# Kernel optimization log

Measured on AMD Instinct MI355X. Metric: run time of the kernel, lower is better.

The kernel has to match this reference:

```python
import jax, jax.numpy as jnp
import numpy as np

N_NODES = 100000

def sage_conv(x, edge_index, W_l, b_l, W_r):
    # PyG SAGEConv (aggr='mean'): out = lin_l(mean_{j in N(i)} x_j) + lin_r(x_i)
    src = edge_index[0]  # message source nodes
    dst = edge_index[1]  # aggregation target nodes
    msgs = x[src]                                   # [E, F] gather
    agg = jax.ops.segment_sum(msgs, dst, num_segments=N_NODES)      # [N, F]
    cnt = jax.ops.segment_sum(jnp.ones((edge_index.shape[1],), x.dtype), dst,
                              num_segments=N_NODES)                 # [N]
    mean = agg / jnp.clip(cnt, 1.0)[:, None]
    return mean @ W_l.T + b_l + x @ W_r.T


def setup_inputs() -> dict:
    key = jax.random.key(0)
    ks = jax.random.split(key, 8)
    num_features, hid, num_classes = 500, 8, 10
    n_edges = 3200000
    x = jax.random.normal(ks[0], (N_NODES, num_features), dtype=jnp.float32)
    edge_index = jax.random.randint(ks[1], (2, n_edges), 0, N_NODES, dtype=jnp.int64)
    def lin(k, fan_in, fan_out):
        bound = 1.0 / np.sqrt(fan_in)
        return jax.random.uniform(k, (fan_out, fan_in), jnp.float32, -bound, bound)
    W1_l = lin(ks[2], num_features, hid)
    b1_l = jax.random.uniform(ks[3], (hid,), jnp.float32, -1/np.sqrt(num_features), 1/np.sqrt(num_features))
    W1_r = lin(ks[4], num_features, hid)
    W2_l = lin(ks[5], hid, num_classes)
    b2_l = jax.random.uniform(ks[6], (num_classes,), jnp.float32, -1/np.sqrt(hid), 1/np.sqrt(hid))
    W2_r = lin(ks[7], hid, num_classes)
    return {"x": x, "edge_index": edge_index,
            "W1_l": W1_l, "b1_l": b1_l, "W1_r": W1_r,
            "W2_l": W2_l, "b2_l": b2_l, "W2_r": W2_r}


def reference(x, edge_index, W1_l, b1_l, W1_r, W2_l, b2_l, W2_r):
    # eval mode: dropout is a no-op
    h = sage_conv(x, edge_index, W1_l, b1_l, W1_r)
    h = jax.nn.elu(h)
    out = sage_conv(h, edge_index, W2_l, b2_l, W2_r)
    return jax.nn.log_softmax(out, axis=1)
```

## Files before the change

### kernel.cpp

```cpp
#include <hip/hip_runtime.h>
#include <hip/hip_bf16.h>
#include <math.h>


#define NBKT_MAX 1600
#define P_BLOCKS 256
#define BSH 6
#define BSZ 64
#define SEG_CAP 4096

typedef float f4v __attribute__((ext_vector_type(4)));
typedef float f32x4 __attribute__((ext_vector_type(4)));
typedef unsigned u32x4 __attribute__((ext_vector_type(4)));
typedef __bf16 bf16x8 __attribute__((ext_vector_type(8)));

__device__ __forceinline__ unsigned f2bf(float f) {
    unsigned u = __float_as_uint(f);
    return (u + 0x7FFFu + ((u >> 16) & 1u)) >> 16;
}
__device__ __forceinline__ float bflo(unsigned w) { return __uint_as_float(w << 16); }
__device__ __forceinline__ float bfhi(unsigned w) { return __uint_as_float(w & 0xFFFF0000u); }

__device__ __forceinline__ unsigned pk2(float lo, float hi) {
    union { __hip_bfloat162 h; unsigned u; } c;
    c.h = __float22bfloat162_rn(make_float2(lo, hi));
    return c.u;
}

__global__ __launch_bounds__(256) void proj1_kernel(
    const float* __restrict__ x,
    const float* __restrict__ W1l,
    const float* __restrict__ W1r,
    unsigned short* __restrict__ yab,
    float* __restrict__ yr,
    int N)
{
    __shared__ __align__(16) unsigned short wls[16 * 520];
    for (int idx = threadIdx.x; idx < 16 * 520; idx += 256) {
        int m = idx / 520, k = idx - m * 520;
        float v = 0.f;
        if (k < 500) v = (m < 8) ? W1l[m * 500 + k] : W1r[(m - 8) * 500 + k];
        wls[idx] = (unsigned short)f2bf(v);
    }
    __syncthreads();

    const int lane = threadIdx.x & 63;
    const int wv   = threadIdx.x >> 6;
    const int tile = blockIdx.x * 4 + wv;
    if (tile * 16 >= N) return;

    const int m  = lane & 15;
    const int kg = lane >> 4;
    const int nodeA = min(tile * 16 + m, N - 1);
    const float* xrow = x + (size_t)nodeA * 500 + kg * 8;
    const unsigned short* wrow = wls + m * 520 + kg * 8;

    union { u32x4 u; bf16x8 b; } af, bf;
    f32x4 acc = {0.f, 0.f, 0.f, 0.f};
    const f4v zero4 = {0.f, 0.f, 0.f, 0.f};

    #pragma unroll 5
    for (int s = 0; s < 15; ++s) {
        f4v xa = *reinterpret_cast<const f4v*>(xrow + s * 32);
        f4v xb = *reinterpret_cast<const f4v*>(xrow + s * 32 + 4);
        af.u.x = pk2(xa.x, xa.y); af.u.y = pk2(xa.z, xa.w);
        af.u.z = pk2(xb.x, xb.y); af.u.w = pk2(xb.z, xb.w);
        bf.b = *reinterpret_cast<const bf16x8*>(wrow + s * 32);
        acc = __builtin_amdgcn_mfma_f32_16x16x32_bf16(af.b, bf.b, acc, 0, 0, 0);
    }
    {
        const int k0 = 480 + kg * 8;
        f4v xa = (k0 + 4 <= 500) ? *reinterpret_cast<const f4v*>(xrow + 480) : zero4;
        f4v xb = (k0 + 8 <= 500) ? *reinterpret_cast<const f4v*>(xrow + 484) : zero4;
        af.u.x = pk2(xa.x, xa.y); af.u.y = pk2(xa.z, xa.w);
        af.u.z = pk2(xb.x, xb.y); af.u.w = pk2(xb.z, xb.w);
        bf.b = *reinterpret_cast<const bf16x8*>(wrow + 480);
        acc = __builtin_amdgcn_mfma_f32_16x16x32_bf16(af.b, bf.b, acc, 0, 0, 0);
    }

    const int ndb = tile * 16 + kg * 4;
    #pragma unroll
    for (int r = 0; r < 4; ++r) {
        int nd = ndb + r;
        if (nd < N) {
            float v = acc[r];
            if (m < 8) yab[(size_t)nd * 8 + m] = (unsigned short)f2bf(v);
            else       yr[(size_t)nd * 8 + (m - 8)] = v;
        }
    }
}

__global__ __launch_bounds__(512) void hist_kernel(
    const int* __restrict__ ei, int E, int chunk, int B,
    int* __restrict__ hist_g)
{
    __shared__ int h[NBKT_MAX];
    for (int i = threadIdx.x; i < B; i += 512) h[i] = 0;
    __syncthreads();
    const int p = blockIdx.x;
    const int e0 = p * chunk, e1 = min(e0 + chunk, E);
    int e = e0 + threadIdx.x;
    for (; e + 512 < e1; e += 1024) {
        int d0 = ei[E + e], d1 = ei[E + e + 512];
        atomicAdd(&h[d0 >> BSH], 1);
        atomicAdd(&h[d1 >> BSH], 1);
    }
    for (; e < e1; e += 512) atomicAdd(&h[ei[E + e] >> BSH], 1);
    __syncthreads();
    for (int b = threadIdx.x; b < B; b += 512)
        hist_g[(size_t)b * P_BLOCKS + p] = h[b];
}

__global__ __launch_bounds__(256) void bsum_kernel(
    const int* __restrict__ hist_g, int* __restrict__ tot)
{
    __shared__ int s[256];
    const int b = blockIdx.x;
    s[threadIdx.x] = hist_g[(size_t)b * P_BLOCKS + threadIdx.x];
    __syncthreads();
    for (int o = 128; o > 0; o >>= 1) {
        if (threadIdx.x < o) s[threadIdx.x] += s[threadIdx.x + o];
        __syncthreads();
    }
    if (threadIdx.x == 0) tot[b] = s[0];
}

__global__ __launch_bounds__(256) void base_kernel(
    int* __restrict__ hist_g, const int* __restrict__ tot, int B,
    int* __restrict__ bstart)
{
    __shared__ int sr[256];
    __shared__ int s2[256];
    __shared__ int bs_sh;
    const int b = blockIdx.x, tid = threadIdx.x;

    int part = 0;
    for (int i = tid; i < b; i += 256) part += tot[i];
    sr[tid] = part;
    __syncthreads();
    for (int o = 128; o > 0; o >>= 1) {
        if (tid < o) sr[tid] += sr[tid + o];
        __syncthreads();
    }
    if (tid == 0) bs_sh = sr[0];
    __syncthreads();
    const int bs = bs_sh;

    const int v = hist_g[(size_t)b * P_BLOCKS + tid];
    s2[tid] = v;
    __syncthreads();
    for (int o = 1; o < 256; o <<= 1) {
        int t = (tid >= o) ? s2[tid - o] : 0;
        __syncthreads();
        s2[tid] += t;
        __syncthreads();
    }
    hist_g[(size_t)b * P_BLOCKS + tid] = bs + s2[tid] - v;
    if (tid == 0) bstart[b] = bs;
    if (b == B - 1 && tid == 255) bstart[B] = bs + s2[255];
}

__global__ __launch_bounds__(512) void scatter2_kernel(
    const int* __restrict__ ei, int E, int chunk, int B,
    const int* __restrict__ base, unsigned* __restrict__ csr)
{
    __shared__ int cur[NBKT_MAX];
    const int p = blockIdx.x;
    for (int b = threadIdx.x; b < B; b += 512) cur[b] = base[(size_t)b * P_BLOCKS + p];
    __syncthreads();
    const int e0 = p * chunk, e1 = min(e0 + chunk, E);
    int e = e0 + threadIdx.x;
    for (; e + 512 < e1; e += 1024) {
        int s0 = ei[e],     s1 = ei[e + 512];
        int d0 = ei[E + e], d1 = ei[E + e + 512];
        int p0 = atomicAdd(&cur[d0 >> BSH], 1);
        int p1 = atomicAdd(&cur[d1 >> BSH], 1);
        csr[p0] = (unsigned)s0 | ((unsigned)(d0 & (BSZ - 1)) << 17);
        csr[p1] = (unsigned)s1 | ((unsigned)(d1 & (BSZ - 1)) << 17);
    }
    for (; e < e1; e += 512) {
        int s0 = ei[e], d0 = ei[E + e];
        int p0 = atomicAdd(&cur[d0 >> BSH], 1);
        csr[p0] = (unsigned)s0 | ((unsigned)(d0 & (BSZ - 1)) << 17);
    }
}

__global__ __launch_bounds__(256) void sortB_kernel(
    const int* __restrict__ bstart,
    unsigned* __restrict__ csr,
    int* __restrict__ nodeoff,
    int B)
{
    __shared__ unsigned stage[SEG_CAP];
    __shared__ int cnt[BSZ];
    __shared__ int cur[BSZ];
    const int b = blockIdx.x, tid = threadIdx.x;
    const int e0 = bstart[b], e1 = bstart[b + 1];
    const int n = e1 - e0;

    if (tid < BSZ) cnt[tid] = 0;
    for (int i = tid; i < n; i += 256) stage[i] = csr[e0 + i];
    __syncthreads();
    for (int i = tid; i < n; i += 256) atomicAdd(&cnt[stage[i] >> 17], 1);
    __syncthreads();
    if (tid < BSZ) {
        int v = cnt[tid];
        int incl = v;
        #pragma unroll
        for (int o = 1; o < 64; o <<= 1) {
            int t = __shfl_up(incl, o);
            if ((tid & 63) >= o) incl += t;
        }
        int excl = e0 + incl - v;
        cur[tid] = excl;
        nodeoff[(size_t)b * BSZ + tid] = excl;
        if (b == B - 1 && tid == 0) nodeoff[(size_t)B * BSZ] = e1;
    }
    __syncthreads();
    for (int i = tid; i < n; i += 256) {
        unsigned pk = stage[i];
        int pos = atomicAdd(&cur[pk >> 17], 1);
        csr[pos] = pk & 0x1FFFFu;
    }
}

__global__ __launch_bounds__(256) void agg1R_kernel(
    const int* __restrict__ nodeoff,
    const unsigned* __restrict__ csr,
    const unsigned short* __restrict__ yab,
    const float* __restrict__ yr,
    const float* __restrict__ b1,
    const float* __restrict__ W2l,
    const float* __restrict__ b2,
    const float* __restrict__ W2r,
    unsigned short* __restrict__ zlb,
    float* __restrict__ zrb,
    int N)
{
    __shared__ float wb[178];
    const int tid = threadIdx.x;
    if (tid < 178)
        wb[tid] = (tid < 8) ? b1[tid] : (tid < 88) ? W2l[tid - 8]
                 : (tid < 98) ? b2[tid - 88] : W2r[tid - 98];
    __syncthreads();

    const int g = tid >> 2;
    const int q = tid & 3;
    const int node = blockIdx.x * BSZ + g;
    const int gs = nodeoff[node], ge = nodeoff[node + 1];
    const uint4* ya4 = reinterpret_cast<const uint4*>(yab);

    float a[8];
    #pragma unroll
    for (int i = 0; i < 8; ++i) a[i] = 0.f;

    for (int e = gs + q; e < ge; e += 4) {
        unsigned s = csr[e];
        uint4 r = ya4[s];
        a[0] += bflo(r.x); a[1] += bfhi(r.x);
        a[2] += bflo(r.y); a[3] += bfhi(r.y);
        a[4] += bflo(r.z); a[5] += bfhi(r.z);
        a[6] += bflo(r.w); a[7] += bfhi(r.w);
    }
    #pragma unroll
    for (int i = 0; i < 8; ++i) {
        a[i] += __shfl_xor(a[i], 1);
        a[i] += __shfl_xor(a[i], 2);
    }

    if (q != 0 || node >= N) return;
    const int deg = ge - gs;
    const float inv = 1.f / fmaxf((float)deg, 1.f);
    const f4v* yr4 = reinterpret_cast<const f4v*>(yr + (size_t)node * 8);
    f4v r0 = yr4[0], r1 = yr4[1];
    const float rr[8] = {r0.x, r0.y, r0.z, r0.w, r1.x, r1.y, r1.z, r1.w};

    float h[8];
    #pragma unroll
    for (int t = 0; t < 8; ++t) {
        float v = a[t] * inv + wb[t] + rr[t];
        h[t] = v > 0.f ? v : expm1f(v);
    }

    float zlv[10], zrv[10];
    #pragma unroll
    for (int k = 0; k < 10; ++k) {
        float al = 0.f, ar = wb[88 + k];
        #pragma unroll
        for (int t = 0; t < 8; ++t) {
            al += wb[8 + k * 8 + t]  * h[t];
            ar += wb[98 + k * 8 + t] * h[t];
        }
        zlv[k] = al; zrv[k] = ar;
    }

    uint4 h0, h1;
    h0.x = f2bf(zlv[0]) | (f2bf(zlv[1]) << 16);
    h0.y = f2bf(zlv[2]) | (f2bf(zlv[3]) << 16);
    h0.z = f2bf(zlv[4]);
    h0.w = 0u;
    h1.x = f2bf(zlv[5]) | (f2bf(zlv[6]) << 16);
    h1.y = f2bf(zlv[7]) | (f2bf(zlv[8]) << 16);
    h1.z = f2bf(zlv[9]);
    h1.w = 0u;
    uint4* zl4w = reinterpret_cast<uint4*>(zlb + (size_t)node * 16);
    zl4w[0] = h0;
    zl4w[1] = h1;

    float4* zr4w = reinterpret_cast<float4*>(zrb + (size_t)node * 12);
    zr4w[0] = make_float4(zrv[0], zrv[1], zrv[2], zrv[3]);
    zr4w[1] = make_float4(zrv[4], zrv[5], zrv[6], zrv[7]);
    zr4w[2] = make_float4(zrv[8], zrv[9], inv, 0.f);
}

__global__ __launch_bounds__(256) void agg2R_kernel(
    const int* __restrict__ nodeoff,
    const unsigned* __restrict__ csr,
    const unsigned short* __restrict__ zlb,
    const float* __restrict__ zrb,
    float* __restrict__ out,
    int N)
{
    const int tid = threadIdx.x;
    const int g = tid >> 2;
    const int q = tid & 3;
    const int node = blockIdx.x * BSZ + g;
    const int gs = nodeoff[node], ge = nodeoff[node + 1];
    const uint4* zl4 = reinterpret_cast<const uint4*>(zlb);

    float a[10];
    #pragma unroll
    for (int i = 0; i < 10; ++i) a[i] = 0.f;

    for (int e = gs + q; e < ge; e += 4) {
        unsigned s = csr[e];
        uint4 rA = zl4[(size_t)s * 2];
        uint4 rB = zl4[(size_t)s * 2 + 1];
        a[0] += bflo(rA.x); a[1] += bfhi(rA.x);
        a[2] += bflo(rA.y); a[3] += bfhi(rA.y);
        a[4] += bflo(rA.z);
        a[5] += bflo(rB.x); a[6] += bfhi(rB.x);
        a[7] += bflo(rB.y); a[8] += bfhi(rB.y);
        a[9] += bflo(rB.z);
    }
    #pragma unroll
    for (int i = 0; i < 10; ++i) {
        a[i] += __shfl_xor(a[i], 1);
        a[i] += __shfl_xor(a[i], 2);
    }

    if (q != 0 || node >= N) return;
    const float* zr = zrb + (size_t)node * 12;
    const float inv = zr[10];
    float v[10];
    float mx = -1e30f;
    #pragma unroll
    for (int k = 0; k < 10; ++k) {
        v[k] = a[k] * inv + zr[k];
        mx = fmaxf(mx, v[k]);
    }
    float ssum = 0.f;
    #pragma unroll
    for (int k = 0; k < 10; ++k) ssum += expf(v[k] - mx);
    const float lse = mx + logf(ssum);
    float2* o = reinterpret_cast<float2*>(out + (size_t)node * 10);
    o[0] = make_float2(v[0] - lse, v[1] - lse);
    o[1] = make_float2(v[2] - lse, v[3] - lse);
    o[2] = make_float2(v[4] - lse, v[5] - lse);
    o[3] = make_float2(v[6] - lse, v[7] - lse);
    o[4] = make_float2(v[8] - lse, v[9] - lse);
}

extern "C" void kernel_launch(void* const* d_in, const int* in_sizes, int n_in,
                              void* d_out, int out_size, void* d_ws, size_t ws_size,
                              hipStream_t stream) {
    const float* x   = (const float*)d_in[0];
    const int*   ei  = (const int*)d_in[1];
    const float* W1l = (const float*)d_in[2];
    const float* b1l = (const float*)d_in[3];
    const float* W1r = (const float*)d_in[4];
    const float* W2l = (const float*)d_in[5];
    const float* b2l = (const float*)d_in[6];
    const float* W2r = (const float*)d_in[7];
    float* out = (float*)d_out;

    const int N = in_sizes[0] / 500;
    const int E = in_sizes[1] / 2;
    const int B = (N + BSZ - 1) >> BSH;
    const int chunk = (E + P_BLOCKS - 1) / P_BLOCKS;
    const int ntiles = (N + 15) / 16;
    const int pblocks = (ntiles + 3) / 4;

    int* hist_g  = (int*)d_ws;
    int* tot     = hist_g + (size_t)B * P_BLOCKS;
    int* bstart  = tot + B;
    int* nodeoff = bstart + (B + 1);
    unsigned* csr = (unsigned*)(nodeoff + (size_t)B * BSZ + 1);
    size_t off = ((char*)(csr + E) - (char*)d_ws + 15) & ~(size_t)15;
    unsigned short* yab = (unsigned short*)((char*)d_ws + off);
    off = (off + (size_t)N * 16 + 15) & ~(size_t)15;
    unsigned short* zlb = (unsigned short*)((char*)d_ws + off);
    off = (off + (size_t)N * 32 + 15) & ~(size_t)15;
    float* yr  = (float*)((char*)d_ws + off);
    float* zrb = yr + (size_t)8 * N;

    proj1_kernel<<<pblocks, 256, 0, stream>>>(x, W1l, W1r, yab, yr, N);
    hist_kernel<<<P_BLOCKS, 512, 0, stream>>>(ei, E, chunk, B, hist_g);
    bsum_kernel<<<B, 256, 0, stream>>>(hist_g, tot);
    base_kernel<<<B, 256, 0, stream>>>(hist_g, tot, B, bstart);
    scatter2_kernel<<<P_BLOCKS, 512, 0, stream>>>(ei, E, chunk, B, hist_g, csr);
    sortB_kernel<<<B, 256, 0, stream>>>(bstart, csr, nodeoff, B);
    agg1R_kernel<<<B, 256, 0, stream>>>(nodeoff, csr, yab, yr, b1l, W2l, b2l, W2r,
                                        zlb, zrb, N);
    agg2R_kernel<<<B, 256, 0, stream>>>(nodeoff, csr, zlb, zrb, out, N);
}
```

Measured before the change: 196.9 us.

## Restructure proj1 as persistent waves staging coalesced x tiles through LDS

The projection kernel becomes a grid-stride persistent kernel with 1024 blocks of two waves. Each wave keeps the packed bf16 weight fragments in registers instead of an LDS copy, then for every 16-node tile loads x rows coalesced across lanes into a per-wave LDS buffer before the MFMA loop reads from it. This targets the strided per-lane row reads of the old version, which read 32-byte pieces from 16 different rows, and drops the per-block weight reload. In exchange it adds an LDS round trip per tile and more register pressure, and the tile loads run serially with no overlap against the compute. There is no barrier between the LDS writes and the MFMA reads, so it relies on the writes being visible within the same wave.

```diff
diff --git a/kernel.cpp b/kernel.cpp
--- a/kernel.cpp
+++ b/kernel.cpp
@@ -8,6 +8,7 @@
 #define BSH 6
 #define BSZ 64
 #define SEG_CAP 4096
+#define PT_ROW 520
 
 typedef float f4v __attribute__((ext_vector_type(4)));
 typedef float f32x4 __attribute__((ext_vector_type(4)));
@@ -27,7 +28,7 @@
     return c.u;
 }
 
-__global__ __launch_bounds__(256) void proj1_kernel(
+__global__ __launch_bounds__(128) void proj1_kernel(
     const float* __restrict__ x,
     const float* __restrict__ W1l,
     const float* __restrict__ W1r,
@@ -35,57 +36,75 @@
     float* __restrict__ yr,
     int N)
 {
-    __shared__ __align__(16) unsigned short wls[16 * 520];
-    for (int idx = threadIdx.x; idx < 16 * 520; idx += 256) {
-        int m = idx / 520, k = idx - m * 520;
-        float v = 0.f;
-        if (k < 500) v = (m < 8) ? W1l[m * 500 + k] : W1r[(m - 8) * 500 + k];
-        wls[idx] = (unsigned short)f2bf(v);
-    }
-    __syncthreads();
-
+    __shared__ __align__(16) unsigned short xls[2][16 * PT_ROW];
     const int lane = threadIdx.x & 63;
     const int wv   = threadIdx.x >> 6;
-    const int tile = blockIdx.x * 4 + wv;
-    if (tile * 16 >= N) return;
-
+    unsigned short* xw = xls[wv];
     const int m  = lane & 15;
     const int kg = lane >> 4;
-    const int nodeA = min(tile * 16 + m, N - 1);
-    const float* xrow = x + (size_t)nodeA * 500 + kg * 8;
-    const unsigned short* wrow = wls + m * 520 + kg * 8;
-
-    union { u32x4 u; bf16x8 b; } af, bf;
-    f32x4 acc = {0.f, 0.f, 0.f, 0.f};
+
+    const float* wrow = (m < 8) ? (W1l + m * 500) : (W1r + (m - 8) * 500);
     const f4v zero4 = {0.f, 0.f, 0.f, 0.f};
-
-    #pragma unroll 5
-    for (int s = 0; s < 15; ++s) {
-        f4v xa = *reinterpret_cast<const f4v*>(xrow + s * 32);
-        f4v xb = *reinterpret_cast<const f4v*>(xrow + s * 32 + 4);
-        af.u.x = pk2(xa.x, xa.y); af.u.y = pk2(xa.z, xa.w);
-        af.u.z = pk2(xb.x, xb.y); af.u.w = pk2(xb.z, xb.w);
-        bf.b = *reinterpret_cast<const bf16x8*>(wrow + s * 32);
-        acc = __builtin_amdgcn_mfma_f32_16x16x32_bf16(af.b, bf.b, acc, 0, 0, 0);
-    }
-    {
-        const int k0 = 480 + kg * 8;
-        f4v xa = (k0 + 4 <= 500) ? *reinterpret_cast<const f4v*>(xrow + 480) : zero4;
-        f4v xb = (k0 + 8 <= 500) ? *reinterpret_cast<const f4v*>(xrow + 484) : zero4;
-        af.u.x = pk2(xa.x, xa.y); af.u.y = pk2(xa.z, xa.w);
-        af.u.z = pk2(xb.x, xb.y); af.u.w = pk2(xb.z, xb.w);
-        bf.b = *reinterpret_cast<const bf16x8*>(wrow + 480);
-        acc = __builtin_amdgcn_mfma_f32_16x16x32_bf16(af.b, bf.b, acc, 0, 0, 0);
-    }
-
-    const int ndb = tile * 16 + kg * 4;
-    #pragma unroll
-    for (int r = 0; r < 4; ++r) {
-        int nd = ndb + r;
-        if (nd < N) {
-            float v = acc[r];
-            if (m < 8) yab[(size_t)nd * 8 + m] = (unsigned short)f2bf(v);
-            else       yr[(size_t)nd * 8 + (m - 8)] = v;
+    u32x4 bq[16];
+    #pragma unroll
+    for (int s = 0; s < 16; ++s) {
+        int k0 = s * 32 + kg * 8;
+        f4v wa = (k0 + 4 <= 500) ? *reinterpret_cast<const f4v*>(wrow + k0) : zero4;
+        f4v wb = (k0 + 8 <= 500) ? *reinterpret_cast<const f4v*>(wrow + k0 + 4) : zero4;
+        bq[s].x = pk2(wa.x, wa.y);
+        bq[s].y = pk2(wa.z, wa.w);
+        bq[s].z = pk2(wb.x, wb.y);
+        bq[s].w = pk2(wb.z, wb.w);
+    }
+
+    const int nt = (N + 15) >> 4;
+    const int gw = blockIdx.x * 2 + wv;
+    const int nw = gridDim.x * 2;
+    const size_t xcap = (size_t)N * 500;
+
+    for (int t = gw; t < nt; t += nw) {
+        const size_t base = (size_t)t * 16 * 500;
+
+        #pragma unroll 4
+        for (int r = 0; r < 16; ++r) {
+            const float* xr = x + base + (size_t)r * 500;
+            uint2* lr = reinterpret_cast<uint2*>(xw + r * PT_ROW);
+            {
+                size_t gi = base + (size_t)r * 500 + (size_t)lane * 4;
+                f4v v = (gi + 4 <= xcap) ? *reinterpret_cast<const f4v*>(xr + lane * 4) : zero4;
+                lr[lane] = make_uint2(pk2(v.x, v.y), pk2(v.z, v.w));
+            }
+            {
+                int i4 = 64 + lane;
+                if (lane < 61) {
+                    size_t gi = base + (size_t)r * 500 + (size_t)i4 * 4;
+                    f4v v = (gi + 4 <= xcap) ? *reinterpret_cast<const f4v*>(xr + i4 * 4) : zero4;
+                    lr[i4] = make_uint2(pk2(v.x, v.y), pk2(v.z, v.w));
+                } else {
+                    lr[i4] = make_uint2(0u, 0u);
+                }
+            }
+        }
+
+        f32x4 acc = {0.f, 0.f, 0.f, 0.f};
+        const unsigned short* ar = xw + m * PT_ROW + kg * 8;
+        #pragma unroll
+        for (int s = 0; s < 16; ++s) {
+            union { u32x4 u; bf16x8 b; } av, bv;
+            av.b = *reinterpret_cast<const bf16x8*>(ar + s * 32);
+            bv.u = bq[s];
+            acc = __builtin_amdgcn_mfma_f32_16x16x32_bf16(av.b, bv.b, acc, 0, 0, 0);
+        }
+
+        const int ndb = t * 16 + kg * 4;
+        #pragma unroll
+        for (int r = 0; r < 4; ++r) {
+            int nd = ndb + r;
+            if (nd < N) {
+                float v = acc[r];
+                if (m < 8) yab[(size_t)nd * 8 + m] = (unsigned short)f2bf(v);
+                else       yr[(size_t)nd * 8 + (m - 8)] = v;
+            }
         }
     }
 }
@@ -388,8 +407,6 @@
     const int E = in_sizes[1] / 2;
     const int B = (N + BSZ - 1) >> BSH;
     const int chunk = (E + P_BLOCKS - 1) / P_BLOCKS;
-    const int ntiles = (N + 15) / 16;
-    const int pblocks = (ntiles + 3) / 4;
 
     int* hist_g  = (int*)d_ws;
     int* tot     = hist_g + (size_t)B * P_BLOCKS;
@@ -404,7 +421,7 @@
     float* yr  = (float*)((char*)d_ws + off);
     float* zrb = yr + (size_t)8 * N;
 
-    proj1_kernel<<<pblocks, 256, 0, stream>>>(x, W1l, W1r, yab, yr, N);
+    proj1_kernel<<<1024, 128, 0, stream>>>(x, W1l, W1r, yab, yr, N);
     hist_kernel<<<P_BLOCKS, 512, 0, stream>>>(ei, E, chunk, B, hist_g);
     bsum_kernel<<<B, 256, 0, stream>>>(hist_g, tot);
     base_kernel<<<B, 256, 0, stream>>>(hist_g, tot, B, bstart);
```

Measured after the change: 206.5 us. 1.05x slower.
